# Kernel optimization log

Hardware: AMD Instinct MI355X
Metric: run time of the kernel (lower is better)

Reference implementation:

```python
import jax, jax.numpy as jnp
import numpy as np
from jax import lax

NUM_CLS = 58

def _bsign(a):
    # BNN sign: +1 for a >= 0, -1 otherwise
    return jnp.where(a >= 0, 1.0, -1.0).astype(a.dtype)

def _conv(x, w, stride=1):
    return lax.conv_general_dilated(
        x, w, window_strides=(stride, stride), padding='VALID',
        dimension_numbers=('NCHW', 'OIHW', 'NCHW'))

def _binconv(x, w):
    # BinaryConv2d: binarize activations and weights via sign, then conv
    return _conv(_bsign(x), _bsign(w))

def _maxpool(x, k=2, s=2):
    return lax.reduce_window(x, -jnp.inf, lax.max,
                             (1, 1, k, k), (1, 1, s, s), 'VALID')

def setup_inputs() -> dict:
    key = jax.random.key(0)
    ks = jax.random.split(key, 7)
    B = 1024
    x = jax.random.normal(ks[0], (B, 3, 32, 32), dtype=jnp.float32)
    w0 = jax.random.normal(ks[1], (128, 3, 3, 3), dtype=jnp.float32) * 0.1   # float conv
    w1 = jax.random.normal(ks[2], (128, 128, 3, 3), dtype=jnp.float32) * 0.1 # binary conv
    w2 = jax.random.normal(ks[3], (128, 128, 3, 3), dtype=jnp.float32) * 0.1 # binary conv
    w3 = jax.random.normal(ks[4], (128, 128, 3, 3), dtype=jnp.float32) * 0.1 # binary conv
    w4 = jax.random.normal(ks[5], (128, 128, 1, 1), dtype=jnp.float32) * 0.1 # binary 1x1
    w5 = jax.random.normal(ks[6], (NUM_CLS, 128, 1, 1), dtype=jnp.float32) * 0.1  # float 1x1
    return {'x': x, 'w0': w0, 'w1': w1, 'w2': w2, 'w3': w3, 'w4': w4, 'w5': w5}

def reference(x, w0, w1, w2, w3, w4, w5):
    # features
    h = _conv(x, w0)            # [B,128,30,30]
    h = _maxpool(h, 2, 2)       # [B,128,15,15]
    h = _binconv(h, w1)         # [B,128,13,13]
    h = _maxpool(h, 2, 2)       # [B,128,6,6]
    h = _binconv(h, w2)         # [B,128,4,4]
    h = _maxpool(h, 2, 1)       # [B,128,3,3]
    # classifier
    h = _binconv(h, w3)         # [B,128,1,1]
    h = _binconv(h, w4)         # [B,128,1,1]
    h = jax.nn.relu(h)
    h = _conv(h, w5)            # [B,58,1,1]
    return jax.nn.softmax(h, axis=1)
```

## Files before the change

### kernel.cpp

```cpp
#include <hip/hip_runtime.h>
#include <cmath>

#define NUM_CLS 58

typedef _Float16 v8h __attribute__((ext_vector_type(8)));
typedef float v4f __attribute__((ext_vector_type(4)));
union HU { v8h h; uint4 u; };

__global__ __launch_bounds__(256) void prep_all(
    const float* __restrict__ w0, const float* __restrict__ w1,
    const float* __restrict__ w2, const float* __restrict__ w3,
    const float* __restrict__ w4,
    unsigned long long* __restrict__ wb1, unsigned long long* __restrict__ wb2,
    unsigned long long* __restrict__ wb3, unsigned long long* __restrict__ wb4,
    _Float16* __restrict__ bsig, _Float16* __restrict__ babs) {
    int id = blockIdx.x, tid = threadIdx.x;
    int lane = tid & 63, wv = tid >> 6;
    if (id < 384) {
        int layer = id >> 7, oc = id & 127;
        const float* w = layer == 0 ? w1 : (layer == 1 ? w2 : w3);
        unsigned long long* o = layer == 0 ? wb1 : (layer == 1 ? wb2 : wb3);
        __shared__ float s[1152];
        const float* base = w + (size_t)oc * 1152;
        for (int i = tid; i < 1152; i += 256) s[i] = base[i];
        __syncthreads();
        for (int k = wv; k < 9; k += 4) {
            unsigned long long b0 = __ballot(s[lane * 9 + k] >= 0.f);
            unsigned long long b1 = __ballot(s[(lane + 64) * 9 + k] >= 0.f);
            if (lane == 0) { o[(oc * 9 + k) * 2] = b0; o[(oc * 9 + k) * 2 + 1] = b1; }
        }
    } else if (id < 416) {
        int oc = (id - 384) * 4 + wv;
        unsigned long long b0 = __ballot(w4[oc * 128 + lane] >= 0.f);
        unsigned long long b1 = __ballot(w4[oc * 128 + lane + 64] >= 0.f);
        if (lane == 0) { wb4[oc * 2] = b0; wb4[oc * 2 + 1] = b1; }
    } else {
        int nt = (id - 416) * 4 + wv;
        int n = nt * 16 + (lane & 15);
        int k0 = (lane >> 4) * 8;
#pragma unroll
        for (int j = 0; j < 8; j++) {
            int k = k0 + j;
            float v = (k < 27) ? w0[n * 27 + k] : 0.f;
            bsig[(nt * 64 + lane) * 8 + j] = (_Float16)v;
            babs[(nt * 64 + lane) * 8 + j] = (_Float16)fabsf(v);
        }
    }
}

__global__ __launch_bounds__(256, 4) void fused_net(
    const float* __restrict__ x, const float* __restrict__ w0,
    const _Float16* __restrict__ bsigG, const _Float16* __restrict__ babsG,
    const unsigned long long* __restrict__ wb1, const unsigned long long* __restrict__ wb2,
    const unsigned long long* __restrict__ wb3, const unsigned long long* __restrict__ wb4,
    const float* __restrict__ w5, float* __restrict__ out) {
    __shared__ _Float16 xh[3172];
    __shared__ uint4 bfrag[512];
    __shared__ uint4 bfraga[512];
    __shared__ alignas(16) unsigned long long bits1[450];
    __shared__ alignas(16) unsigned long long bits2[72];
    __shared__ unsigned long long bits3[18];
    __shared__ unsigned long long bits4[2];
    __shared__ float r_s[128];
    __shared__ float l_s[NUM_CLS];
    __shared__ float e_s[NUM_CLS];
    __shared__ unsigned int qcnt;
    __shared__ unsigned int queue[256];

    int b = blockIdx.x;
    int tid = threadIdx.x;
    int lane = tid & 63, wave = tid >> 6;
    const float* xb = x + (size_t)b * 3072;

    {
        for (int i = tid; i < 3072; i += 256) {
            int c = i >> 10, rem = i & 1023;
            xh[c * 1057 + (rem >> 5) * 33 + (rem & 31)] = (_Float16)xb[i];
        }
        const uint4* bs4 = (const uint4*)bsigG;
        const uint4* ba4 = (const uint4*)babsG;
        for (int i = tid; i < 512; i += 256) { bfrag[i] = bs4[i]; bfraga[i] = ba4[i]; }
        if (tid == 0) qcnt = 0;

        int k0 = (lane >> 4) * 8;
        int offj[8];
#pragma unroll
        for (int j = 0; j < 8; j++) {
            int k = k0 + j;
            int c = k / 9, r = (k % 9) / 3, q = k % 3;
            offj[j] = c * 1057 + r * 33 + q;
        }
        unsigned short* b1u16 = (unsigned short*)bits1;
        __syncthreads();

        for (int mt = wave; mt < 57; mt += 4) {
            int mg = mt * 16 + (lane & 15);
            int me = mg < 900 ? mg : 899;
            int p = me >> 2, win = me & 3;
            int py = p / 15, px = p - py * 15;
            int base = (py * 2 + (win >> 1)) * 33 + px * 2 + (win & 1);
            v8h a;
#pragma unroll
            for (int j = 0; j < 8; j++)
                a[j] = (k0 + j < 27) ? xh[base + offj[j]] : (_Float16)0.f;
            HU ua; ua.h = a;
            ua.u.x &= 0x7FFF7FFFu; ua.u.y &= 0x7FFF7FFFu;
            ua.u.z &= 0x7FFF7FFFu; ua.u.w &= 0x7FFF7FFFu;
            int myp = mt * 4 + (lane >> 4);
#pragma unroll
            for (int nt = 0; nt < 8; nt++) {
                HU bs; bs.u = bfrag[nt * 64 + lane];
                HU ba; ba.u = bfraga[nt * 64 + lane];
                v4f s  = __builtin_amdgcn_mfma_f32_16x16x32_f16(a,    bs.h, (v4f){0.f,0.f,0.f,0.f}, 0, 0, 0);
                v4f sa = __builtin_amdgcn_mfma_f32_16x16x32_f16(ua.h, ba.h, (v4f){0.f,0.f,0.f,0.f}, 0, 0, 0);
                float bd0 = fmaf(sa[0], 1.1e-3f, 1e-5f);
                float bd1 = fmaf(sa[1], 1.1e-3f, 1e-5f);
                float bd2 = fmaf(sa[2], 1.1e-3f, 1e-5f);
                float bd3 = fmaf(sa[3], 1.1e-3f, 1e-5f);
                unsigned long long mkpos =
                    __ballot(s[0] >= bd0) | __ballot(s[1] >= bd1) |
                    __ballot(s[2] >= bd2) | __ballot(s[3] >= bd3);
                unsigned long long mkunc =
                    (__ballot(fabsf(s[0]) < bd0) | __ballot(fabsf(s[1]) < bd1) |
                     __ballot(fabsf(s[2]) < bd2) | __ballot(fabsf(s[3]) < bd3)) & ~mkpos;
                if ((lane & 15) == 0 && myp < 225)
                    b1u16[myp * 8 + nt] = (unsigned short)(mkpos >> (lane & 48));
                if (__builtin_expect(mkunc != 0ull, 0)) {
                    if (((mkunc >> lane) & 1ull) && myp < 225) {
                        unsigned int qi = atomicAdd(&qcnt, 1u);
                        if (qi < 256) queue[qi] = (unsigned)myp | ((unsigned)(nt * 16 + (lane & 15)) << 8);
                    }
                }
            }
        }
        __syncthreads();
        unsigned int nq = qcnt < 256u ? qcnt : 256u;
        for (unsigned int i = tid; i < nq; i += 256) {
            unsigned int e = queue[i];
            int p = e & 255; int oc = (e >> 8) & 255;
            int py = p / 15, px = p - py * 15;
            bool pos = false;
#pragma unroll
            for (int win = 0; win < 4; win++) {
                int base = (py * 2 + (win >> 1)) * 32 + px * 2 + (win & 1);
                double sd = 0.0;
#pragma unroll
                for (int k = 0; k < 27; k++) {
                    int c = k / 9, r = (k % 9) / 3, q = k % 3;
                    sd += (double)xb[base + c * 1024 + r * 32 + q] * (double)w0[oc * 27 + k];
                }
                pos |= (sd >= 0.0);
            }
            if (pos) atomicOr(&bits1[p * 2 + (oc >> 6)], 1ull << (oc & 63));
        }
    }
    __syncthreads();

    int wave2 = tid >> 6, half = wave2 & 1, pair = wave2 >> 1;
    int oc = half * 64 + lane;

    {
        unsigned long long wr[18];
#pragma unroll
        for (int j = 0; j < 18; j++) wr[j] = wb1[oc * 18 + j];
        const ulonglong2* b1v = (const ulonglong2*)bits1;
        for (int p = pair; p < 36; p += 2) {
            int py = p / 6, px = p % 6;
            int P0 = 0, P1 = 0, P2 = 0, P3 = 0;
#pragma unroll
            for (int yy = 0; yy < 4; yy++) {
                int rb = (2 * py + yy) * 15 + 2 * px;
                ulonglong2 q0 = b1v[rb];
                ulonglong2 q1 = b1v[rb + 1];
                ulonglong2 q2 = b1v[rb + 2];
                ulonglong2 q3 = b1v[rb + 3];
#pragma unroll
                for (int dy = 0; dy < 2; dy++) {
                    int ky = yy - dy;
                    if (ky < 0 || ky > 2) continue;
#pragma unroll
                    for (int kx = 0; kx < 3; kx++) {
                        ulonglong2 qa = kx == 0 ? q0 : (kx == 1 ? q1 : q2);
                        ulonglong2 qb = kx == 0 ? q1 : (kx == 1 ? q2 : q3);
                        int d0 = __popcll(qa.x ^ wr[(ky * 3 + kx) * 2]) +
                                 __popcll(qa.y ^ wr[(ky * 3 + kx) * 2 + 1]);
                        int d1 = __popcll(qb.x ^ wr[(ky * 3 + kx) * 2]) +
                                 __popcll(qb.y ^ wr[(ky * 3 + kx) * 2 + 1]);
                        if (dy == 0) { P0 += d0; P1 += d1; }
                        else         { P2 += d0; P3 += d1; }
                    }
                }
            }
            unsigned long long m = __ballot(P0 <= 576) | __ballot(P1 <= 576) |
                                   __ballot(P2 <= 576) | __ballot(P3 <= 576);
            if (lane == 0) bits2[p * 2 + half] = m;
        }
    }
    __syncthreads();

    {
        unsigned long long wr[18];
#pragma unroll
        for (int j = 0; j < 18; j++) wr[j] = wb2[oc * 18 + j];
        const ulonglong2* b2v = (const ulonglong2*)bits2;
        for (int p = pair; p < 9; p += 2) {
            int py = p / 3, px = p % 3;
            int P4[4];
#pragma unroll
            for (int dy = 0; dy < 2; dy++)
#pragma unroll
                for (int dx = 0; dx < 2; dx++) {
                    int P = 0;
#pragma unroll
                    for (int ky = 0; ky < 3; ky++)
#pragma unroll
                        for (int kx = 0; kx < 3; kx++) {
                            ulonglong2 q = b2v[(py + dy + ky) * 6 + (px + dx + kx)];
                            P += __popcll(q.x ^ wr[(ky * 3 + kx) * 2]);
                            P += __popcll(q.y ^ wr[(ky * 3 + kx) * 2 + 1]);
                        }
                    P4[dy * 2 + dx] = P;
                }
            unsigned long long m = __ballot(P4[0] <= 576) | __ballot(P4[1] <= 576) |
                                   __ballot(P4[2] <= 576) | __ballot(P4[3] <= 576);
            if (lane == 0) bits3[p * 2 + half] = m;
        }
    }
    __syncthreads();

    if (tid < 128) {
        int P = 0;
#pragma unroll
        for (int k = 0; k < 9; k++) {
            P += __popcll(bits3[k * 2] ^ wb3[tid * 18 + k * 2]);
            P += __popcll(bits3[k * 2 + 1] ^ wb3[tid * 18 + k * 2 + 1]);
        }
        unsigned long long m = __ballot(P <= 576);
        if ((tid & 63) == 0) bits4[tid >> 6] = m;
    }
    __syncthreads();
    if (tid < 128) {
        unsigned long long i0 = bits4[0], i1 = bits4[1];
        int v = 128 - 2 * (int)(__popcll(i0 ^ wb4[tid * 2]) + __popcll(i1 ^ wb4[tid * 2 + 1]));
        r_s[tid] = v > 0 ? (float)v : 0.f;
    }
    __syncthreads();
    if (tid < NUM_CLS) {
        float l = 0.f;
#pragma unroll 8
        for (int k = 0; k < 128; k++) l = fmaf(w5[tid * 128 + k], r_s[k], l);
        l_s[tid] = l;
    }
    __syncthreads();
    if (tid < NUM_CLS) {
        float mx = -1e30f;
        for (int k = 0; k < NUM_CLS; k++) mx = fmaxf(mx, l_s[k]);
        e_s[tid] = expf(l_s[tid] - mx);
    }
    __syncthreads();
    if (tid < NUM_CLS) {
        float sum = 0.f;
        for (int k = 0; k < NUM_CLS; k++) sum += e_s[k];
        out[(size_t)b * NUM_CLS + tid] = e_s[tid] / sum;
    }
}

extern "C" void kernel_launch(void* const* d_in, const int* in_sizes, int n_in,
                              void* d_out, int out_size, void* d_ws, size_t ws_size,
                              hipStream_t stream) {
    const float* x  = (const float*)d_in[0];
    const float* w0 = (const float*)d_in[1];
    const float* w1 = (const float*)d_in[2];
    const float* w2 = (const float*)d_in[3];
    const float* w3 = (const float*)d_in[4];
    const float* w4 = (const float*)d_in[5];
    const float* w5 = (const float*)d_in[6];
    float* out = (float*)d_out;

    int B = in_sizes[0] / 3072;

    size_t off = 0;
    auto carve = [&](size_t bytes) {
        void* p = (char*)d_ws + off;
        off += (bytes + 255) & ~(size_t)255;
        return p;
    };
    unsigned long long* wb1 = (unsigned long long*)carve(1152 * 2 * 8);
    unsigned long long* wb2 = (unsigned long long*)carve(1152 * 2 * 8);
    unsigned long long* wb3 = (unsigned long long*)carve(1152 * 2 * 8);
    unsigned long long* wb4 = (unsigned long long*)carve(128 * 2 * 8);
    _Float16* bsig = (_Float16*)carve(8 * 64 * 8 * 2);
    _Float16* babs = (_Float16*)carve(8 * 64 * 8 * 2);
    (void)ws_size; (void)n_in; (void)out_size;

    prep_all<<<418, 256, 0, stream>>>(w0, w1, w2, w3, w4, wb1, wb2, wb3, wb4, bsig, babs);
    fused_net<<<B, 256, 0, stream>>>(x, w0, bsig, babs, wb1, wb2, wb3, wb4, w5, out);
}
```

Measured before the change: 159.9 us.

## Split fused network into half-channel conv0 kernel and separate tail kernel

The first float conv plus maxpool and sign stage moves into its own kernel. That kernel is launched with two blocks per image, each handling 64 of the 128 output channels, and writes the packed sign bits to a global workspace. A second kernel reads those bits and runs the binary layers and the classifier. The aim is more parallelism and lower shared memory per block for the MFMA-heavy first stage, at the cost of an extra launch, a global round trip for the bits, and loading the input image twice.

```diff
diff --git a/kernel.cpp b/kernel.cpp
--- a/kernel.cpp
+++ b/kernel.cpp
@@ -48,15 +48,115 @@
     }
 }
 
-__global__ __launch_bounds__(256, 4) void fused_net(
+__global__ __launch_bounds__(256, 4) void conv0_half(
     const float* __restrict__ x, const float* __restrict__ w0,
     const _Float16* __restrict__ bsigG, const _Float16* __restrict__ babsG,
+    unsigned long long* __restrict__ bits1G) {
+    __shared__ _Float16 xh[3172];
+    __shared__ uint4 bfrag[256];
+    __shared__ uint4 bfraga[256];
+    __shared__ alignas(16) unsigned long long bits1h[225];
+    __shared__ unsigned int qcnt;
+    __shared__ unsigned int queue[256];
+
+    int bid = blockIdx.x;
+    int b = bid >> 1, half = bid & 1;
+    int tid = threadIdx.x;
+    int lane = tid & 63, wave = tid >> 6;
+    const float* xb = x + (size_t)b * 3072;
+
+    for (int i = tid; i < 3072; i += 256) {
+        int c = i >> 10, rem = i & 1023;
+        xh[c * 1057 + (rem >> 5) * 33 + (rem & 31)] = (_Float16)xb[i];
+    }
+    const uint4* bs4 = (const uint4*)bsigG + half * 256;
+    const uint4* ba4 = (const uint4*)babsG + half * 256;
+    if (tid < 256) { bfrag[tid] = bs4[tid]; bfraga[tid] = ba4[tid]; }
+    if (tid == 0) qcnt = 0;
+
+    int col = lane & 15;
+    int k0 = (lane >> 4) * 8;
+    int offj[8];
+#pragma unroll
+    for (int j = 0; j < 8; j++) {
+        int k = k0 + j;
+        int c = k / 9, r = (k % 9) / 3, q = k % 3;
+        offj[j] = c * 1057 + r * 33 + q;
+    }
+    unsigned short* b1u16 = (unsigned short*)bits1h;
+    __syncthreads();
+
+    for (int mt = wave; mt < 57; mt += 4) {
+        int mg = mt * 16 + col;
+        int me = mg < 900 ? mg : 899;
+        int p = me >> 2, win = me & 3;
+        int py = p / 15, px = p - py * 15;
+        int base = (py * 2 + (win >> 1)) * 33 + px * 2 + (win & 1);
+        v8h a;
+#pragma unroll
+        for (int j = 0; j < 8; j++)
+            a[j] = (k0 + j < 27) ? xh[base + offj[j]] : (_Float16)0.f;
+        HU ua; ua.h = a;
+        ua.u.x &= 0x7FFF7FFFu; ua.u.y &= 0x7FFF7FFFu;
+        ua.u.z &= 0x7FFF7FFFu; ua.u.w &= 0x7FFF7FFFu;
+        int myp = mt * 4 + (lane >> 4);
+#pragma unroll
+        for (int ntl = 0; ntl < 4; ntl++) {
+            HU bs; bs.u = bfrag[ntl * 64 + lane];
+            HU ba; ba.u = bfraga[ntl * 64 + lane];
+            v4f s  = __builtin_amdgcn_mfma_f32_16x16x32_f16(a,    bs.h, (v4f){0.f,0.f,0.f,0.f}, 0, 0, 0);
+            v4f sa = __builtin_amdgcn_mfma_f32_16x16x32_f16(ua.h, ba.h, (v4f){0.f,0.f,0.f,0.f}, 0, 0, 0);
+            float bd0 = fmaf(sa[0], 1.1e-3f, 1e-5f);
+            float bd1 = fmaf(sa[1], 1.1e-3f, 1e-5f);
+            float bd2 = fmaf(sa[2], 1.1e-3f, 1e-5f);
+            float bd3 = fmaf(sa[3], 1.1e-3f, 1e-5f);
+            unsigned long long mkpos =
+                __ballot(s[0] >= bd0) | __ballot(s[1] >= bd1) |
+                __ballot(s[2] >= bd2) | __ballot(s[3] >= bd3);
+            unsigned long long mkunc =
+                (__ballot(fabsf(s[0]) < bd0) | __ballot(fabsf(s[1]) < bd1) |
+                 __ballot(fabsf(s[2]) < bd2) | __ballot(fabsf(s[3]) < bd3)) & ~mkpos;
+            if ((lane & 15) == 0 && myp < 225)
+                b1u16[myp * 4 + ntl] = (unsigned short)(mkpos >> (lane & 48));
+            if (__builtin_expect(mkunc != 0ull, 0)) {
+                if (((mkunc >> lane) & 1ull) && myp < 225) {
+                    unsigned int qi = atomicAdd(&qcnt, 1u);
+                    if (qi < 256) queue[qi] = (unsigned)myp | ((unsigned)(ntl * 16 + col) << 8);
+                }
+            }
+        }
+    }
+    __syncthreads();
+    unsigned int nq = qcnt < 256u ? qcnt : 256u;
+    for (unsigned int i = tid; i < nq; i += 256) {
+        unsigned int e = queue[i];
+        int p = e & 255; int ocl = (e >> 8) & 255;
+        int oc = half * 64 + ocl;
+        int py = p / 15, px = p - py * 15;
+        bool pos = false;
+#pragma unroll
+        for (int win = 0; win < 4; win++) {
+            int base = (py * 2 + (win >> 1)) * 32 + px * 2 + (win & 1);
+            double sd = 0.0;
+#pragma unroll
+            for (int k = 0; k < 27; k++) {
+                int c = k / 9, r = (k % 9) / 3, q = k % 3;
+                sd += (double)xb[base + c * 1024 + r * 32 + q] * (double)w0[oc * 27 + k];
+            }
+            pos |= (sd >= 0.0);
+        }
+        if (pos) atomicOr(&bits1h[p], 1ull << ocl);
+    }
+    __syncthreads();
+    unsigned long long* dst = bits1G + (size_t)(b * 2 + half) * 225;
+    for (int i = tid; i < 225; i += 256) dst[i] = bits1h[i];
+}
+
+__global__ __launch_bounds__(256, 4) void tail_net(
+    const unsigned long long* __restrict__ bits1G,
     const unsigned long long* __restrict__ wb1, const unsigned long long* __restrict__ wb2,
     const unsigned long long* __restrict__ wb3, const unsigned long long* __restrict__ wb4,
     const float* __restrict__ w5, float* __restrict__ out) {
-    __shared__ _Float16 xh[3172];
-    __shared__ uint4 bfrag[512];
-    __shared__ uint4 bfraga[512];
     __shared__ alignas(16) unsigned long long bits1[450];
     __shared__ alignas(16) unsigned long long bits2[72];
     __shared__ unsigned long long bits3[18];
@@ -64,94 +164,15 @@
     __shared__ float r_s[128];
     __shared__ float l_s[NUM_CLS];
     __shared__ float e_s[NUM_CLS];
-    __shared__ unsigned int qcnt;
-    __shared__ unsigned int queue[256];
 
     int b = blockIdx.x;
     int tid = threadIdx.x;
-    int lane = tid & 63, wave = tid >> 6;
-    const float* xb = x + (size_t)b * 3072;
-
+    int lane = tid & 63;
     {
-        for (int i = tid; i < 3072; i += 256) {
-            int c = i >> 10, rem = i & 1023;
-            xh[c * 1057 + (rem >> 5) * 33 + (rem & 31)] = (_Float16)xb[i];
-        }
-        const uint4* bs4 = (const uint4*)bsigG;
-        const uint4* ba4 = (const uint4*)babsG;
-        for (int i = tid; i < 512; i += 256) { bfrag[i] = bs4[i]; bfraga[i] = ba4[i]; }
-        if (tid == 0) qcnt = 0;
-
-        int k0 = (lane >> 4) * 8;
-        int offj[8];
-#pragma unroll
-        for (int j = 0; j < 8; j++) {
-            int k = k0 + j;
-            int c = k / 9, r = (k % 9) / 3, q = k % 3;
-            offj[j] = c * 1057 + r * 33 + q;
-        }
-        unsigned short* b1u16 = (unsigned short*)bits1;
-        __syncthreads();
-
-        for (int mt = wave; mt < 57; mt += 4) {
-            int mg = mt * 16 + (lane & 15);
-            int me = mg < 900 ? mg : 899;
-            int p = me >> 2, win = me & 3;
-            int py = p / 15, px = p - py * 15;
-            int base = (py * 2 + (win >> 1)) * 33 + px * 2 + (win & 1);
-            v8h a;
-#pragma unroll
-            for (int j = 0; j < 8; j++)
-                a[j] = (k0 + j < 27) ? xh[base + offj[j]] : (_Float16)0.f;
-            HU ua; ua.h = a;
-            ua.u.x &= 0x7FFF7FFFu; ua.u.y &= 0x7FFF7FFFu;
-            ua.u.z &= 0x7FFF7FFFu; ua.u.w &= 0x7FFF7FFFu;
-            int myp = mt * 4 + (lane >> 4);
-#pragma unroll
-            for (int nt = 0; nt < 8; nt++) {
-                HU bs; bs.u = bfrag[nt * 64 + lane];
-                HU ba; ba.u = bfraga[nt * 64 + lane];
-                v4f s  = __builtin_amdgcn_mfma_f32_16x16x32_f16(a,    bs.h, (v4f){0.f,0.f,0.f,0.f}, 0, 0, 0);
-                v4f sa = __builtin_amdgcn_mfma_f32_16x16x32_f16(ua.h, ba.h, (v4f){0.f,0.f,0.f,0.f}, 0, 0, 0);
-                float bd0 = fmaf(sa[0], 1.1e-3f, 1e-5f);
-                float bd1 = fmaf(sa[1], 1.1e-3f, 1e-5f);
-                float bd2 = fmaf(sa[2], 1.1e-3f, 1e-5f);
-                float bd3 = fmaf(sa[3], 1.1e-3f, 1e-5f);
-                unsigned long long mkpos =
-                    __ballot(s[0] >= bd0) | __ballot(s[1] >= bd1) |
-                    __ballot(s[2] >= bd2) | __ballot(s[3] >= bd3);
-                unsigned long long mkunc =
-                    (__ballot(fabsf(s[0]) < bd0) | __ballot(fabsf(s[1]) < bd1) |
-                     __ballot(fabsf(s[2]) < bd2) | __ballot(fabsf(s[3]) < bd3)) & ~mkpos;
-                if ((lane & 15) == 0 && myp < 225)
-                    b1u16[myp * 8 + nt] = (unsigned short)(mkpos >> (lane & 48));
-                if (__builtin_expect(mkunc != 0ull, 0)) {
-                    if (((mkunc >> lane) & 1ull) && myp < 225) {
-                        unsigned int qi = atomicAdd(&qcnt, 1u);
-                        if (qi < 256) queue[qi] = (unsigned)myp | ((unsigned)(nt * 16 + (lane & 15)) << 8);
-                    }
-                }
-            }
-        }
-        __syncthreads();
-        unsigned int nq = qcnt < 256u ? qcnt : 256u;
-        for (unsigned int i = tid; i < nq; i += 256) {
-            unsigned int e = queue[i];
-            int p = e & 255; int oc = (e >> 8) & 255;
-            int py = p / 15, px = p - py * 15;
-            bool pos = false;
-#pragma unroll
-            for (int win = 0; win < 4; win++) {
-                int base = (py * 2 + (win >> 1)) * 32 + px * 2 + (win & 1);
-                double sd = 0.0;
-#pragma unroll
-                for (int k = 0; k < 27; k++) {
-                    int c = k / 9, r = (k % 9) / 3, q = k % 3;
-                    sd += (double)xb[base + c * 1024 + r * 32 + q] * (double)w0[oc * 27 + k];
-                }
-                pos |= (sd >= 0.0);
-            }
-            if (pos) atomicOr(&bits1[p * 2 + (oc >> 6)], 1ull << (oc & 63));
+        const unsigned long long* src = bits1G + (size_t)b * 450;
+        for (int i = tid; i < 450; i += 256) {
+            int half = i >= 225, p = i - half * 225;
+            bits1[p * 2 + half] = src[i];
         }
     }
     __syncthreads();
@@ -291,8 +312,10 @@
     unsigned long long* wb4 = (unsigned long long*)carve(128 * 2 * 8);
     _Float16* bsig = (_Float16*)carve(8 * 64 * 8 * 2);
     _Float16* babs = (_Float16*)carve(8 * 64 * 8 * 2);
+    unsigned long long* bits1G = (unsigned long long*)carve((size_t)B * 450 * 8);
     (void)ws_size; (void)n_in; (void)out_size;
 
     prep_all<<<418, 256, 0, stream>>>(w0, w1, w2, w3, w4, wb1, wb2, wb3, wb4, bsig, babs);
-    fused_net<<<B, 256, 0, stream>>>(x, w0, bsig, babs, wb1, wb2, wb3, wb4, w5, out);
+    conv0_half<<<B * 2, 256, 0, stream>>>(x, w0, bsig, babs, bits1G);
+    tail_net<<<B, 256, 0, stream>>>(bits1G, wb1, wb2, wb3, wb4, w5, out);
 }
```

New measurement: 174.5 us. +9.1%, slower.
